# Kernel optimization log

Hardware: AMD Instinct MI355X
Metric: run time of the kernel (lower is better)

The kernel has to match this reference:

```python
import jax, jax.numpy as jnp
import numpy as np

B, S, D = 2, 1024, 7168
H, HD, RD, QL = 64, 128, 64, 1536
EPS = 1e-6
SOFTMAX_SCALE = HD ** (-0.5)


def _rope_interleave(x, cos, sin):
    """Interleaved RoPE (pairs x[2i], x[2i+1]); x: [T, n, RD], cos/sin: [T, RD]."""
    x1 = x[..., 0::2]
    x2 = x[..., 1::2]
    c = cos[:, None, 0::2]
    s = sin[:, None, 0::2]
    o1 = x1 * c - x2 * s
    o2 = x2 * c + x1 * s
    return jnp.stack([o1, o2], axis=-1).reshape(x.shape)


def setup_inputs() -> dict:
    key = jax.random.key(0)
    ks = jax.random.split(key, 8)
    x = jax.random.normal(ks[0], (B, S, D), dtype=jnp.float32) * 0.02
    qr = jax.random.normal(ks[1], (B * S, QL), dtype=jnp.float32) * 0.02
    # real interleaved-RoPE cos/sin tables, tiled over batch
    pos = jnp.arange(S, dtype=jnp.float32)
    inv_freq = 1.0 / (10000.0 ** (jnp.arange(0, RD, 2, dtype=jnp.float32) / RD))
    freqs = pos[:, None] * inv_freq[None, :]                      # [S, RD/2]
    cos = jnp.repeat(jnp.cos(freqs), 2, axis=-1)                  # [S, RD]
    sin = jnp.repeat(jnp.sin(freqs), 2, axis=-1)
    cos = jnp.tile(cos, (B, 1))                                   # [B*S, RD]
    sin = jnp.tile(sin, (B, 1))
    wq_b_w = jax.random.normal(ks[2], (QL, H * HD), dtype=jnp.float32) * (QL ** -0.5)
    wk_w = jax.random.normal(ks[3], (D, HD), dtype=jnp.float32) * (D ** -0.5)
    wproj_w = jax.random.normal(ks[4], (D, H), dtype=jnp.float32) * (D ** -0.5)
    ln_gamma = jnp.ones((HD,), dtype=jnp.float32)
    ln_beta = jnp.ones((HD,), dtype=jnp.float32)  # module inits bias to ones
    return {"x": x, "qr": qr, "cos": cos, "sin": sin, "wq_b_w": wq_b_w,
            "wk_w": wk_w, "wproj_w": wproj_w, "ln_gamma": ln_gamma, "ln_beta": ln_beta}


def reference(x, qr, cos, sin, wq_b_w, wk_w, wproj_w, ln_gamma, ln_beta):
    b, s, d = x.shape
    t = b * s
    xf = x.reshape(t, d)
    # ---- query path: low-rank up-proj, split rope/nope, interleaved RoPE ----
    q = (qr @ wq_b_w).reshape(t, H, HD)
    q_pe, q_nope = q[..., :RD], q[..., RD:]
    q_pe = _rope_interleave(q_pe, cos, sin)
    q = jnp.concatenate([q_pe, q_nope], axis=-1).reshape(b, s, H, HD)
    # ---- per-head gating weights ----
    w = (xf @ wproj_w).reshape(b, s, H)
    # ---- key path: project, LayerNorm, RoPE on rope slice ----
    kp = xf @ wk_w                                                # [T, HD]
    mu = jnp.mean(kp, axis=-1, keepdims=True)
    var = jnp.mean(jnp.square(kp - mu), axis=-1, keepdims=True)
    kn = (kp - mu) * jax.lax.rsqrt(var + EPS) * ln_gamma + ln_beta
    k_pe, k_nope = kn[..., :RD], kn[..., RD:]
    k_pe = _rope_interleave(k_pe[:, None, :], cos, sin)[:, 0]
    k = jnp.concatenate([k_pe, k_nope], axis=-1).reshape(b, s, HD)
    # ---- lightning-indexer scores: weighted ReLU(q.k) summed over heads ----
    logits = jnp.einsum("bqhd,bkd->bqhk", q, k)                   # [B,S,H,S]
    scores = SOFTMAX_SCALE * jnp.einsum("bqh,bqhk->bqk", w, jax.nn.relu(logits))
    return scores
```

## Files before the change

### kernel.cpp

```cpp
#include <hip/hip_runtime.h>

typedef unsigned short u16;
typedef unsigned int   u32;

typedef __bf16 bf16x8 __attribute__((ext_vector_type(8)));
typedef float  f32x4  __attribute__((ext_vector_type(4)));

__device__ __forceinline__ float bf2f(u16 u){ u32 x = ((u32)u) << 16; return __builtin_bit_cast(float, x); }
__device__ __forceinline__ u16 f2bf(float f){
  u32 u = __builtin_bit_cast(u32, f);
  u32 r = (u + 0x7FFFu + ((u >> 16) & 1u)) >> 16;
  return (u16)r;
}
__device__ __forceinline__ u32 pk2bf(float a, float b){
  u32 ua = __builtin_bit_cast(u32, a) + 0x8000u;
  u32 ub = __builtin_bit_cast(u32, b) + 0x8000u;
  return __builtin_amdgcn_perm(ub, ua, 0x07060302u);
}
__device__ __forceinline__ void glds16(const void* g, void* l){
  __builtin_amdgcn_global_load_lds((const __attribute__((address_space(1))) void*)g,
                                   (__attribute__((address_space(3))) void*)l, 16, 0, 0);
}
__device__ __forceinline__ void hard_barrier(){
  asm volatile("" ::: "memory");
  __builtin_amdgcn_s_barrier();
  asm volatile("" ::: "memory");
}

__global__ __launch_bounds__(256) void transpose_f32_bf16_v(const float* __restrict__ src,
                                                            u16* __restrict__ dst, int R, int C){
  __shared__ u16 T[64 * 72];
  int c0 = blockIdx.x * 64, r0 = blockIdx.y * 64;
  int tr  = threadIdx.x >> 3;
  int tc8 = (threadIdx.x & 7) * 8;
  #pragma unroll
  for (int it = 0; it < 2; ++it){
    int rr = tr + it * 32;
    const float* sp = src + (size_t)(r0 + rr) * C + c0 + tc8;
    float4 f0 = *(const float4*)sp, f1 = *(const float4*)(sp + 4);
    u16 v[8] = { f2bf(f0.x), f2bf(f0.y), f2bf(f0.z), f2bf(f0.w),
                 f2bf(f1.x), f2bf(f1.y), f2bf(f1.z), f2bf(f1.w) };
    #pragma unroll
    for (int j = 0; j < 8; ++j) T[(tc8 + j) * 72 + rr] = v[j];
  }
  __syncthreads();
  int tcw = threadIdx.x >> 3;
  int tr8 = (threadIdx.x & 7) * 8;
  #pragma unroll
  for (int it = 0; it < 2; ++it){
    int cc = tcw + it * 32;
    *(uint4*)(dst + (size_t)(c0 + cc) * R + r0 + tr8) = *(const uint4*)&T[cc * 72 + tr8];
  }
}

__global__ __launch_bounds__(256) void cvt_f32_bf16(const float* __restrict__ src,
                                                    u16* __restrict__ dst){
  size_t i = ((size_t)blockIdx.x * 256 + threadIdx.x) * 8;
  const float4* a4 = (const float4*)(src + i);
  float4 f0 = a4[0], f1 = a4[1];
  u32 w[4] = { pk2bf(f0.x, f0.y), pk2bf(f0.z, f0.w), pk2bf(f1.x, f1.y), pk2bf(f1.z, f1.w) };
  *(uint4*)(dst + i) = *(const uint4*)w;
}

__global__ __launch_bounds__(256) void proj_splitk(const float* __restrict__ X,
    const u16* __restrict__ BT, float* __restrict__ P){
  constexpr int Kf = 7168;
  const int s = blockIdx.x, m0 = blockIdx.y * 64;
  const int kbase = s * 448;
  __shared__ u16 As[2 * 64 * 36];
  __shared__ u16 Bs[2 * 192 * 32];
  const int tid = threadIdx.x, wave = tid >> 6, lane = tid & 63;
  const int row = lane & 15, quad = lane >> 4;
  const int wm = (wave & 1) * 32, wn = (wave >> 1) * 96;

  const f32x4 zero = {0.f, 0.f, 0.f, 0.f};
  f32x4 acc[2][6];
  #pragma unroll
  for (int mt = 0; mt < 2; ++mt)
    #pragma unroll
    for (int nt = 0; nt < 6; ++nt) acc[mt][nt] = zero;

  for (int kb = 0; kb < 7; ++kb) {
    int k0 = kbase + kb * 64;
    #pragma unroll
    for (int c = 0; c < 6; ++c) {
      int chunk = wave * 6 + c;
      int kc = chunk / 12, rem = chunk % 12;
      int r = rem * 16 + (lane >> 2), col = (lane & 3) * 8;
      glds16(BT + (size_t)r * Kf + k0 + kc * 32 + col, (void*)&Bs[chunk * 512]);
    }
    #pragma unroll
    for (int c = 0; c < 2; ++c) {
      int idx = tid + c * 256;
      int r = idx >> 3, kf = (idx & 7) * 8;
      const float4* ap = (const float4*)(X + (size_t)(m0 + r) * Kf + k0 + kf);
      float4 f0 = ap[0], f1 = ap[1];
      u32 w[4] = { pk2bf(f0.x, f0.y), pk2bf(f0.z, f0.w), pk2bf(f1.x, f1.y), pk2bf(f1.z, f1.w) };
      *(uint4*)&As[(kf >> 5) * 2304 + r * 36 + (kf & 31)] = *(const uint4*)w;
    }
    __syncthreads();
    #pragma unroll
    for (int ks = 0; ks < 2; ++ks) {
      bf16x8 af[2], bfr[6];
      #pragma unroll
      for (int mt = 0; mt < 2; ++mt) af[mt] = *(const bf16x8*)&As[ks * 2304 + (wm + mt * 16 + row) * 36 + quad * 8];
      #pragma unroll
      for (int nt = 0; nt < 6; ++nt) bfr[nt] = *(const bf16x8*)&Bs[ks * 6144 + (wn + nt * 16 + row) * 32 + quad * 8];
      #pragma unroll
      for (int mt = 0; mt < 2; ++mt)
        #pragma unroll
        for (int nt = 0; nt < 6; ++nt)
          acc[mt][nt] = __builtin_amdgcn_mfma_f32_16x16x32_bf16(af[mt], bfr[nt], acc[mt][nt], 0, 0, 0);
    }
    __syncthreads();
  }
  #pragma unroll
  for (int mt = 0; mt < 2; ++mt)
    #pragma unroll
    for (int nt = 0; nt < 6; ++nt)
      #pragma unroll
      for (int r = 0; r < 4; ++r) {
        int rr = m0 + wm + mt * 16 + quad * 4 + r;
        int cc = wn + nt * 16 + row;
        P[((size_t)s * 2048 + rr) * 192 + cc] = acc[mt][nt][r];
      }
}

__global__ __launch_bounds__(64) void reduce_lnrope(const float* __restrict__ P,
    const float* __restrict__ cosb, const float* __restrict__ sinb,
    const float* __restrict__ gam, const float* __restrict__ bet,
    u16* __restrict__ Kout, float* __restrict__ WoutT){
  int tok = blockIdx.x, lane = threadIdx.x;
  float v0 = 0.f, v1 = 0.f, w = 0.f;
  #pragma unroll
  for (int s = 0; s < 16; ++s) {
    const float* p = P + ((size_t)s * 2048 + tok) * 192;
    v0 += p[2 * lane]; v1 += p[2 * lane + 1]; w += p[128 + lane];
  }
  WoutT[(size_t)lane * 2048 + tok] = w;
  float sm = v0 + v1;
  #pragma unroll
  for (int m = 1; m < 64; m <<= 1) sm += __shfl_xor(sm, m);
  float mu = sm * (1.f / 128.f);
  float d0 = v0 - mu, d1 = v1 - mu;
  float sq = d0 * d0 + d1 * d1;
  #pragma unroll
  for (int m = 1; m < 64; m <<= 1) sq += __shfl_xor(sq, m);
  float rs = rsqrtf(sq * (1.f / 128.f) + 1e-6f);
  float kn0 = d0 * rs * gam[2 * lane]     + bet[2 * lane];
  float kn1 = d1 * rs * gam[2 * lane + 1] + bet[2 * lane + 1];
  float o0 = kn0, o1 = kn1;
  if (lane < 32) {
    float c  = cosb[tok * 64 + 2 * lane];
    float sn = sinb[tok * 64 + 2 * lane];
    o0 = kn0 * c - kn1 * sn;
    o1 = kn1 * c + kn0 * sn;
  }
  Kout[tok * 128 + 2 * lane]     = f2bf(o0);
  Kout[tok * 128 + 2 * lane + 1] = f2bf(o1);
}

template<bool AGLDS>
__global__ __launch_bounds__(256) void qgemm(const void* __restrict__ Aptr,
    const u16* __restrict__ BT, const float* __restrict__ cosb,
    const float* __restrict__ sinb, u16* __restrict__ Qout){
  constexpr int K = 1536, N = 8192;
  __shared__ u16 As[2 * 128 * 32];
  __shared__ u16 Bs[2 * 128 * 32];
  const int tid = threadIdx.x, wave = tid >> 6, lane = tid & 63;
  const int row = lane & 15, quad = lane >> 4;
  const int wm = (wave >> 1) * 64, wn = (wave & 1) * 64;
  const int m0 = blockIdx.y * 128, n0 = blockIdx.x * 128;

  const f32x4 zero = {0.f, 0.f, 0.f, 0.f};
  f32x4 acc[4][4];
  #pragma unroll
  for (int mt = 0; mt < 4; ++mt)
    #pragma unroll
    for (int nt = 0; nt < 4; ++nt) acc[mt][nt] = zero;

  for (int k0 = 0; k0 < K; k0 += 64) {
    #pragma unroll
    for (int c = 0; c < 4; ++c) {
      int chunk = wave * 4 + c;
      int kc = chunk >> 3, rg = chunk & 7;
      int r = rg * 16 + (lane >> 2), col = kc * 32 + (lane & 3) * 8;
      glds16(BT + (size_t)(n0 + r) * K + k0 + col, (void*)&Bs[chunk * 512]);
    }
    if (AGLDS) {
      #pragma unroll
      for (int c = 0; c < 4; ++c) {
        int chunk = wave * 4 + c;
        int kc = chunk >> 3, rg = chunk & 7;
        int r = rg * 16 + (lane >> 2), col = kc * 32 + (lane & 3) * 8;
        glds16((const u16*)Aptr + (size_t)(m0 + r) * K + k0 + col, (void*)&As[chunk * 512]);
      }
    } else {
      #pragma unroll
      for (int c = 0; c < 4; ++c) {
        int idx = tid + c * 256;
        int r = idx >> 3, kf = (idx & 7) * 8;
        const float4* ap = (const float4*)((const float*)Aptr + (size_t)(m0 + r) * K + k0 + kf);
        float4 f0 = ap[0], f1 = ap[1];
        u32 w[4] = { pk2bf(f0.x, f0.y), pk2bf(f0.z, f0.w), pk2bf(f1.x, f1.y), pk2bf(f1.z, f1.w) };
        *(uint4*)&As[(kf >> 5) * 4096 + r * 32 + (kf & 31)] = *(const uint4*)w;
      }
    }
    __syncthreads();
    #pragma unroll
    for (int kk = 0; kk < 2; ++kk) {
      bf16x8 af[4], bfr[4];
      #pragma unroll
      for (int mt = 0; mt < 4; ++mt) af[mt]  = *(const bf16x8*)&As[kk * 4096 + (wm + mt * 16 + row) * 32 + quad * 8];
      #pragma unroll
      for (int nt = 0; nt < 4; ++nt) bfr[nt] = *(const bf16x8*)&Bs[kk * 4096 + (wn + nt * 16 + row) * 32 + quad * 8];
      #pragma unroll
      for (int mt = 0; mt < 4; ++mt)
        #pragma unroll
        for (int nt = 0; nt < 4; ++nt)
          acc[mt][nt] = __builtin_amdgcn_mfma_f32_16x16x32_bf16(af[mt], bfr[nt], acc[mt][nt], 0, 0, 0);
    }
    __syncthreads();
  }

  const bool roped = (wn == 0);
  #pragma unroll
  for (int mt = 0; mt < 4; ++mt)
    #pragma unroll
    for (int nt = 0; nt < 4; ++nt)
      #pragma unroll
      for (int r = 0; r < 4; ++r) {
        int rr = m0 + wm + mt * 16 + quad * 4 + r;
        int cc = n0 + wn + nt * 16 + row;
        float v = acc[mt][nt][r];
        float o = v;
        if (roped) {
          int hd = (wn + nt * 16 + row) & 127;
          float c = cosb[rr * 64 + hd];
          float s = sinb[rr * 64 + hd];
          float vo = __shfl_xor(v, 1);
          o = (cc & 1) ? (v * c + vo * s) : (v * c - vo * s);
        }
        Qout[(size_t)rr * N + cc] = f2bf(o);
      }
}

__global__ __launch_bounds__(512, 2) void qgemm256v3(const u16* __restrict__ A,
    const u16* __restrict__ BT, const float* __restrict__ cosb,
    const float* __restrict__ sinb, u16* __restrict__ Qout){
  constexpr int K = 1536, N = 8192, NT = 24;
  __shared__ __align__(16) u16 Asb[2][16384];
  __shared__ __align__(16) u16 Bsb[2][16384];
  const int tid = threadIdx.x, wave = tid >> 6, lane = tid & 63;
  const int lrow = lane & 15, quad = lane >> 4;
  const int wm2 = wave >> 2, wn4 = wave & 3;

  const int flat = blockIdx.y * 32 + blockIdx.x;
  const int n_t  = (flat & 7) * 4 + ((flat >> 3) >> 3);
  const int m_t  = (flat >> 3) & 7;
  const int m0 = m_t * 256, n0 = n_t * 256;

  const int colb = ((lane & 7) << 4) ^ ((lane & 8) << 3) ^ ((lane & 16) << 1) ^ ((lane & 32) >> 1);
  const int cole = colb >> 1;
  const int sub  = lane >> 3;
  const u16* pa[4];
  const u16* pb[4];
  #pragma unroll
  for (int c = 0; c < 4; ++c) {
    int g = wave * 4 + c;
    pa[c] = A  + (size_t)(m0 + g * 8 + sub) * K + cole;
    pb[c] = BT + (size_t)(n0 + g * 8 + sub) * K + cole;
  }
  auto stage = [&](int t, int buf){
    int koff = t * 64;
    #pragma unroll
    for (int c = 0; c < 4; ++c)
      glds16(pa[c] + koff, (void*)&Asb[buf][(wave * 4 + c) * 512]);
    #pragma unroll
    for (int c = 0; c < 4; ++c)
      glds16(pb[c] + koff, (void*)&Bsb[buf][(wave * 4 + c) * 512]);
  };

  const int swz = ((lrow & 1) << 6) | ((lrow & 2) << 4) | ((lrow & 4) << 2);
  const int aob = (wm2 * 128 + lrow) * 128 + quad * 16;
  const int bob = (wn4 * 64  + lrow) * 128 + quad * 16;

  const f32x4 zero = {0.f, 0.f, 0.f, 0.f};
  f32x4 acc[8][4];
  #pragma unroll
  for (int mt = 0; mt < 8; ++mt)
    #pragma unroll
    for (int nt = 0; nt < 4; ++nt) acc[mt][nt] = zero;

  stage(0, 0);
  asm volatile("s_waitcnt vmcnt(0)" ::: "memory");
  hard_barrier();

  for (int t = 0; t < NT; ++t) {
    if (t + 1 < NT) stage(t + 1, (t + 1) & 1);
    const char* Ab = (const char*)&Asb[t & 1][0];
    const char* Bb = (const char*)&Bsb[t & 1][0];
    #pragma unroll 1
    for (int kk = 0; kk < 2; ++kk) {
      bf16x8 af[8], bfr[4];
      #pragma unroll
      for (int mt = 0; mt < 8; ++mt)
        af[mt]  = *(const bf16x8*)(Ab + ((aob + mt * 2048 + kk * 64) ^ swz));
      #pragma unroll
      for (int nt = 0; nt < 4; ++nt)
        bfr[nt] = *(const bf16x8*)(Bb + ((bob + nt * 2048 + kk * 64) ^ swz));
      #pragma unroll
      for (int mt = 0; mt < 8; ++mt)
        #pragma unroll
        for (int nt = 0; nt < 4; ++nt)
          acc[mt][nt] = __builtin_amdgcn_mfma_f32_16x16x32_bf16(af[mt], bfr[nt], acc[mt][nt], 0, 0, 0);
    }
    asm volatile("s_waitcnt vmcnt(0)" ::: "memory");
    hard_barrier();
  }

  const bool roped = !(wn4 & 1);
  #pragma unroll
  for (int mt = 0; mt < 8; ++mt)
    #pragma unroll
    for (int nt = 0; nt < 4; ++nt)
      #pragma unroll
      for (int r = 0; r < 4; ++r) {
        int rr = m0 + wm2 * 128 + mt * 16 + quad * 4 + r;
        int cc = n0 + wn4 * 64 + nt * 16 + lrow;
        float v = acc[mt][nt][r];
        float o = v;
        if (roped) {
          int hd = nt * 16 + lrow;
          float c = cosb[rr * 64 + hd];
          float s = sinb[rr * 64 + hd];
          float vo = __shfl_xor(v, 1);
          o = (cc & 1) ? (v * c + vo * s) : (v * c - vo * s);
        }
        Qout[(size_t)rr * N + cc] = f2bf(o);
      }
}

__global__ __launch_bounds__(256) void attn_kernel(const u16* __restrict__ Q,
    const u16* __restrict__ Kb, const float* __restrict__ WT, float* __restrict__ out){
  int blk = blockIdx.x;
  int x = blk & 7, kt = (blk >> 3) & 7, hs = (blk >> 6) & 1, g4 = (blk >> 7) & 3;
  int p = x + 8 * g4;
  int b = p >> 4, qt = p & 15;
  int q0 = qt * 64, k0 = kt * 128;

  const int tid = threadIdx.x, wave = tid >> 6, lane = tid & 63;
  const int row = lane & 15, quad = lane >> 4;
  const int wm = (wave >> 1) * 32;
  const int wn = (wave & 1) * 64;

  __shared__ u16 Sh[2][16384];
  __shared__ float Ws[32 * 64];

  #pragma unroll
  for (int c = 0; c < 8; ++c) {
    int g = wave * 8 + c;
    int rr = g * 4 + (lane >> 4), col = (lane & 15) * 8;
    glds16(Kb + (size_t)(b * 1024 + k0 + rr) * 128 + col, (void*)&Sh[0][g * 512]);
  }
  {
    int hl = tid >> 3, qq = (tid & 7) * 8;
    const float* srcw = WT + (size_t)(hs * 32 + hl) * 2048 + b * 1024 + q0 + qq;
    *(float4*)&Ws[hl * 64 + qq]     = *(const float4*)srcw;
    *(float4*)&Ws[hl * 64 + qq + 4] = *(const float4*)(srcw + 4);
  }
  __syncthreads();

  bf16x8 bfr[4][4];
  #pragma unroll
  for (int ks = 0; ks < 4; ++ks)
    #pragma unroll
    for (int nt = 0; nt < 4; ++nt)
      bfr[ks][nt] = *(const bf16x8*)&Sh[0][(wn + nt * 16 + row) * 128 + ks * 32 + quad * 8];
  __syncthreads();

  const u16* Qbase = Q + (size_t)(b * 1024 + q0) * 8192;
  auto stage = [&](int half, int pairIdx){
    int h0 = hs * 32 + pairIdx * 2;
    #pragma unroll
    for (int c = 0; c < 8; ++c) {
      int g = wave * 8 + c;
      int hsub = g >> 4, rem = g & 15;
      int kc = rem >> 2, rg = rem & 3;
      glds16(Qbase + (size_t)(rg * 16 + (lane >> 2)) * 8192 + (h0 + hsub) * 128 + kc * 32 + (lane & 3) * 8,
             (void*)&Sh[half][hsub * 8192 + rem * 512]);
    }
  };

  const f32x4 zero = {0.f, 0.f, 0.f, 0.f};
  f32x4 sacc[2][4];
  #pragma unroll
  for (int mt = 0; mt < 2; ++mt)
    #pragma unroll
    for (int nt = 0; nt < 4; ++nt) sacc[mt][nt] = zero;

  stage(0, 0);
  for (int hp = 0; hp < 16; ++hp) {
    __syncthreads();
    if (hp < 15) stage((hp + 1) & 1, hp + 1);
    const u16* S = Sh[hp & 1];
    #pragma unroll
    for (int hsub = 0; hsub < 2; ++hsub) {
      f32x4 lg[2][4];
      #pragma unroll
      for (int mt = 0; mt < 2; ++mt)
        #pragma unroll
        for (int nt = 0; nt < 4; ++nt) lg[mt][nt] = zero;
      #pragma unroll
      for (int ks = 0; ks < 4; ++ks) {
        bf16x8 af0 = *(const bf16x8*)&S[hsub * 8192 + ks * 2048 + (wm +      row) * 32 + quad * 8];
        bf16x8 af1 = *(const bf16x8*)&S[hsub * 8192 + ks * 2048 + (wm + 16 + row) * 32 + quad * 8];
        #pragma unroll
        for (int nt = 0; nt < 4; ++nt) {
          lg[0][nt] = __builtin_amdgcn_mfma_f32_16x16x32_bf16(af0, bfr[ks][nt], lg[0][nt], 0, 0, 0);
          lg[1][nt] = __builtin_amdgcn_mfma_f32_16x16x32_bf16(af1, bfr[ks][nt], lg[1][nt], 0, 0, 0);
        }
      }
      int hl = hp * 2 + hsub;
      f32x4 w0 = *(const f32x4*)&Ws[hl * 64 + wm +      quad * 4];
      f32x4 w1 = *(const f32x4*)&Ws[hl * 64 + wm + 16 + quad * 4];
      #pragma unroll
      for (int nt = 0; nt < 4; ++nt)
        #pragma unroll
        for (int r = 0; r < 4; ++r) {
          sacc[0][nt][r] += w0[r] * fmaxf(lg[0][nt][r], 0.f);
          sacc[1][nt][r] += w1[r] * fmaxf(lg[1][nt][r], 0.f);
        }
    }
  }

  const float scale = 0.088388347648318447f;
  #pragma unroll
  for (int mt = 0; mt < 2; ++mt)
    #pragma unroll
    for (int nt = 0; nt < 4; ++nt)
      #pragma unroll
      for (int r = 0; r < 4; ++r) {
        int qq = q0 + wm + mt * 16 + quad * 4 + r;
        int kk = k0 + wn + nt * 16 + row;
        unsafeAtomicAdd(&out[((size_t)b << 20) + (size_t)qq * 1024 + kk], scale * sacc[mt][nt][r]);
      }
}

extern "C" void kernel_launch(void* const* d_in, const int* in_sizes, int n_in,
                              void* d_out, int out_size, void* d_ws, size_t ws_size,
                              hipStream_t stream) {
  const float* x    = (const float*)d_in[0];
  const float* qr   = (const float*)d_in[1];
  const float* cosb = (const float*)d_in[2];
  const float* sinb = (const float*)d_in[3];
  const float* wq   = (const float*)d_in[4];
  const float* wk   = (const float*)d_in[5];
  const float* wp   = (const float*)d_in[6];
  const float* gam  = (const float*)d_in[7];
  const float* bet  = (const float*)d_in[8];
  float* out = (float*)d_out;

  char* ws = (char*)d_ws;
  float* P    = (float*)(ws + 0);
  u16*   wqT  = (u16*)(ws + 0);
  u16*   wkwpT= (u16*)(ws + 25165824);
  float* WT   = (float*)(ws + 27918336);
  u16*   Kbf  = (u16*)(ws + 28442624);
  u16*   Qbf  = (u16*)(ws + 28966912);
  const size_t QRB_OFF = 62521344;
  u16*   qrb  = (u16*)(ws + QRB_OFF);
  const bool big_ws = (ws_size >= (size_t)68812800);

  (void)in_sizes; (void)n_in;

  hipMemsetAsync(d_out, 0, (size_t)out_size * 4, stream);

  transpose_f32_bf16_v<<<dim3(2, 112), 256, 0, stream>>>(wk, wkwpT,              7168, 128);
  transpose_f32_bf16_v<<<dim3(1, 112), 256, 0, stream>>>(wp, wkwpT + 128 * 7168, 7168, 64);

  proj_splitk<<<dim3(16, 32), 256, 0, stream>>>(x, wkwpT, P);
  reduce_lnrope<<<2048, 64, 0, stream>>>(P, cosb, sinb, gam, bet, Kbf, WT);

  transpose_f32_bf16_v<<<dim3(128, 24), 256, 0, stream>>>(wq, wqT, 1536, 8192);

  if (big_ws) {
    cvt_f32_bf16<<<1536, 256, 0, stream>>>(qr, qrb);
    qgemm256v3<<<dim3(32, 8), 512, 0, stream>>>(qrb, wqT, cosb, sinb, Qbf);
  } else {
    qgemm<false><<<dim3(64, 16), 256, 0, stream>>>(qr, wqT, cosb, sinb, Qbf);
  }

  attn_kernel<<<512, 256, 0, stream>>>(Qbf, Kbf, WT, out);
}
```

Measured before the change: 316.3 us.

## Pipeline Q GEMM with half-tile staging, partial vmcnt waits and MFMA priority

Rewrites the Q up-projection GEMM main loop to stage each 64-wide K tile as two 32-wide halves. Loads are issued one half-tile ahead and waited on with partial vmcnt counts instead of a full drain each iteration. Fragment loads are split so half of the A fragments feed MFMAs while the rest load, and MFMA sections run at raised wave priority. The goal is to hide global-to-LDS latency and barrier stalls, at the cost of more complex wait-count bookkeeping and a new LDS swizzle that must stay bank-conflict free.

```diff
diff --git a/kernel.cpp b/kernel.cpp
--- a/kernel.cpp
+++ b/kernel.cpp
@@ -245,45 +245,42 @@
       }
 }
 
-__global__ __launch_bounds__(512, 2) void qgemm256v3(const u16* __restrict__ A,
+__global__ __launch_bounds__(512, 2) void qgemm256v4(const u16* __restrict__ A,
     const u16* __restrict__ BT, const float* __restrict__ cosb,
     const float* __restrict__ sinb, u16* __restrict__ Qout){
   constexpr int K = 1536, N = 8192, NT = 24;
-  __shared__ __align__(16) u16 Asb[2][16384];
-  __shared__ __align__(16) u16 Bsb[2][16384];
+  __shared__ __align__(16) u16 As[2 * 2 * 256 * 32];
+  __shared__ __align__(16) u16 Bs[2 * 2 * 256 * 32];
   const int tid = threadIdx.x, wave = tid >> 6, lane = tid & 63;
   const int lrow = lane & 15, quad = lane >> 4;
   const int wm2 = wave >> 2, wn4 = wave & 3;
 
   const int flat = blockIdx.y * 32 + blockIdx.x;
-  const int n_t  = (flat & 7) * 4 + ((flat >> 3) >> 3);
+  const int n_t  = (flat & 7) * 4 + (flat >> 6);
   const int m_t  = (flat >> 3) & 7;
   const int m0 = m_t * 256, n0 = n_t * 256;
 
-  const int colb = ((lane & 7) << 4) ^ ((lane & 8) << 3) ^ ((lane & 16) << 1) ^ ((lane & 32) >> 1);
-  const int cole = colb >> 1;
-  const int sub  = lane >> 3;
-  const u16* pa[4];
-  const u16* pb[4];
-  #pragma unroll
-  for (int c = 0; c < 4; ++c) {
-    int g = wave * 4 + c;
-    pa[c] = A  + (size_t)(m0 + g * 8 + sub) * K + cole;
-    pb[c] = BT + (size_t)(n0 + g * 8 + sub) * K + cole;
-  }
-  auto stage = [&](int t, int buf){
-    int koff = t * 64;
-    #pragma unroll
-    for (int c = 0; c < 4; ++c)
-      glds16(pa[c] + koff, (void*)&Asb[buf][(wave * 4 + c) * 512]);
-    #pragma unroll
-    for (int c = 0; c < 4; ++c)
-      glds16(pb[c] + koff, (void*)&Bsb[buf][(wave * 4 + c) * 512]);
+  const int scolb = ((tid & 3) << 4) ^ (((tid >> 3) & 1) << 5) ^ (((tid >> 4) & 1) << 4);
+  const int scole = scolb >> 1;
+  const int srow  = tid >> 2;
+  const u16* sa0 = A  + (size_t)(m0 +       srow) * K + scole;
+  const u16* sa1 = A  + (size_t)(m0 + 128 + srow) * K + scole;
+  const u16* sb0 = BT + (size_t)(n0 +       srow) * K + scole;
+  const u16* sb1 = BT + (size_t)(n0 + 128 + srow) * K + scole;
+
+  auto stagept = [&](int t, int h){
+    const int off = t * 64 + h * 32;
+    u16* la = (u16*)As + (size_t)((t & 1) * 2 + h) * 8192 + wave * 512;
+    u16* lb = (u16*)Bs + (size_t)((t & 1) * 2 + h) * 8192 + wave * 512;
+    glds16(sa0 + off, (void*)la);
+    glds16(sa1 + off, (void*)(la + 4096));
+    glds16(sb0 + off, (void*)lb);
+    glds16(sb1 + off, (void*)(lb + 4096));
   };
 
-  const int swz = ((lrow & 1) << 6) | ((lrow & 2) << 4) | ((lrow & 4) << 2);
-  const int aob = (wm2 * 128 + lrow) * 128 + quad * 16;
-  const int bob = (wn4 * 64  + lrow) * 128 + quad * 16;
+  const int swzr = ((lrow & 2) << 4) | ((lrow & 4) << 2);
+  const int aoff = (wm2 * 128 + lrow) * 64 + ((quad * 16) ^ swzr);
+  const int boff = (wn4 * 64  + lrow) * 64 + ((quad * 16) ^ swzr);
 
   const f32x4 zero = {0.f, 0.f, 0.f, 0.f};
   f32x4 acc[8][4];
@@ -292,31 +289,76 @@
     #pragma unroll
     for (int nt = 0; nt < 4; ++nt) acc[mt][nt] = zero;
 
-  stage(0, 0);
-  asm volatile("s_waitcnt vmcnt(0)" ::: "memory");
-  hard_barrier();
+  stagept(0, 0); stagept(0, 1); stagept(1, 0);
 
   for (int t = 0; t < NT; ++t) {
-    if (t + 1 < NT) stage(t + 1, (t + 1) & 1);
-    const char* Ab = (const char*)&Asb[t & 1][0];
-    const char* Bb = (const char*)&Bsb[t & 1][0];
-    #pragma unroll 1
-    for (int kk = 0; kk < 2; ++kk) {
-      bf16x8 af[8], bfr[4];
-      #pragma unroll
-      for (int mt = 0; mt < 8; ++mt)
-        af[mt]  = *(const bf16x8*)(Ab + ((aob + mt * 2048 + kk * 64) ^ swz));
+    const int d = t & 1;
+    const bool last = (t == NT - 1);
+    const char* A0 = (const char*)As + d * 32768;
+    const char* B0 = (const char*)Bs + d * 32768;
+    const char* A1 = A0 + 16384;
+    const char* B1 = B0 + 16384;
+    bf16x8 af[4], bfr[4];
+
+    if (!last) { asm volatile("s_waitcnt vmcnt(8)" ::: "memory"); }
+    else       { asm volatile("s_waitcnt vmcnt(4)" ::: "memory"); }
+    hard_barrier();
+    #pragma unroll
+    for (int j = 0; j < 4; ++j) af[j]  = *(const bf16x8*)(A0 + aoff + j * 1024);
+    #pragma unroll
+    for (int j = 0; j < 4; ++j) bfr[j] = *(const bf16x8*)(B0 + boff + j * 1024);
+    if (t + 1 < NT) stagept(t + 1, 1);
+    asm volatile("s_waitcnt lgkmcnt(0)" ::: "memory");
+    __builtin_amdgcn_sched_barrier(0);
+    __builtin_amdgcn_s_setprio(1);
+    #pragma unroll
+    for (int j = 0; j < 4; ++j)
       #pragma unroll
       for (int nt = 0; nt < 4; ++nt)
-        bfr[nt] = *(const bf16x8*)(Bb + ((bob + nt * 2048 + kk * 64) ^ swz));
-      #pragma unroll
-      for (int mt = 0; mt < 8; ++mt)
-        #pragma unroll
-        for (int nt = 0; nt < 4; ++nt)
-          acc[mt][nt] = __builtin_amdgcn_mfma_f32_16x16x32_bf16(af[mt], bfr[nt], acc[mt][nt], 0, 0, 0);
-    }
-    asm volatile("s_waitcnt vmcnt(0)" ::: "memory");
+        acc[j][nt] = __builtin_amdgcn_mfma_f32_16x16x32_bf16(af[j], bfr[nt], acc[j][nt], 0, 0, 0);
+    __builtin_amdgcn_s_setprio(0);
+
+    #pragma unroll
+    for (int j = 0; j < 4; ++j) af[j] = *(const bf16x8*)(A0 + aoff + (4 + j) * 1024);
+    asm volatile("s_waitcnt lgkmcnt(0)" ::: "memory");
+    __builtin_amdgcn_sched_barrier(0);
+    __builtin_amdgcn_s_setprio(1);
+    #pragma unroll
+    for (int j = 0; j < 4; ++j)
+      #pragma unroll
+      for (int nt = 0; nt < 4; ++nt)
+        acc[4 + j][nt] = __builtin_amdgcn_mfma_f32_16x16x32_bf16(af[j], bfr[nt], acc[4 + j][nt], 0, 0, 0);
+    __builtin_amdgcn_s_setprio(0);
+
+    if (!last) { asm volatile("s_waitcnt vmcnt(8)" ::: "memory"); }
+    else       { asm volatile("s_waitcnt vmcnt(0)" ::: "memory"); }
     hard_barrier();
+    #pragma unroll
+    for (int j = 0; j < 4; ++j) af[j]  = *(const bf16x8*)(A1 + aoff + j * 1024);
+    #pragma unroll
+    for (int j = 0; j < 4; ++j) bfr[j] = *(const bf16x8*)(B1 + boff + j * 1024);
+    if (t + 2 < NT) stagept(t + 2, 0);
+    asm volatile("s_waitcnt lgkmcnt(0)" ::: "memory");
+    __builtin_amdgcn_sched_barrier(0);
+    __builtin_amdgcn_s_setprio(1);
+    #pragma unroll
+    for (int j = 0; j < 4; ++j)
+      #pragma unroll
+      for (int nt = 0; nt < 4; ++nt)
+        acc[j][nt] = __builtin_amdgcn_mfma_f32_16x16x32_bf16(af[j], bfr[nt], acc[j][nt], 0, 0, 0);
+    __builtin_amdgcn_s_setprio(0);
+
+    #pragma unroll
+    for (int j = 0; j < 4; ++j) af[j] = *(const bf16x8*)(A1 + aoff + (4 + j) * 1024);
+    asm volatile("s_waitcnt lgkmcnt(0)" ::: "memory");
+    __builtin_amdgcn_sched_barrier(0);
+    __builtin_amdgcn_s_setprio(1);
+    #pragma unroll
+    for (int j = 0; j < 4; ++j)
+      #pragma unroll
+      for (int nt = 0; nt < 4; ++nt)
+        acc[4 + j][nt] = __builtin_amdgcn_mfma_f32_16x16x32_bf16(af[j], bfr[nt], acc[4 + j][nt], 0, 0, 0);
+    __builtin_amdgcn_s_setprio(0);
   }
 
   const bool roped = !(wn4 & 1);
@@ -486,7 +528,7 @@
 
   if (big_ws) {
     cvt_f32_bf16<<<1536, 256, 0, stream>>>(qr, qrb);
-    qgemm256v3<<<dim3(32, 8), 512, 0, stream>>>(qrb, wqT, cosb, sinb, Qbf);
+    qgemm256v4<<<dim3(32, 8), 512, 0, stream>>>(qrb, wqT, cosb, sinb, Qbf);
   } else {
     qgemm<false><<<dim3(64, 16), 256, 0, stream>>>(qr, wqT, cosb, sinb, Qbf);
   }
```

New measurement: 305.2 us. -3.5%, faster.
